# Performance work log

Hardware: AMD Instinct MI355X
Metric: run time of the kernel (lower is better)

## Reference

```python
import jax, jax.numpy as jnp
import numpy as np

K = 5  # kNN neighbors (includes self, as in PyG knn(x, x, k))


def _lin_bn(x, W, b, s, h):
    # Linear -> ReLU -> BatchNorm (inference, folded to scale s / shift h)
    return jax.nn.relu(x @ W + b) * s + h


def _knn_idx(x, k):
    # x: [B, N, F] -> idx: [B, N, k] indices of k nearest points (incl. self)
    x2 = jnp.sum(x * x, axis=-1)  # [B, N]
    d = x2[:, :, None] + x2[:, None, :] - 2.0 * jnp.einsum('bnf,bmf->bnm', x, x)
    return jax.lax.top_k(-d, k)[1]


def _edge_conv(x, k, edge_mlp):
    # DynamicEdgeConv: knn graph, message mlp([x_i, x_j - x_i]), max-aggregate
    idx = _knn_idx(x, k)                                   # [B, N, k]
    xj = jax.vmap(lambda xb, ib: xb[ib])(x, idx)           # [B, N, k, F]
    xi = jnp.broadcast_to(x[:, :, None, :], xj.shape)
    e = jnp.concatenate([xi, xj - xi], axis=-1)            # [B, N, k, 2F]
    return jnp.max(edge_mlp(e), axis=2)                    # [B, N, F_out]


def _forward(pos, w1a, b1a, s1a, h1a, w1b, b1b, s1b, h1b, w1c, b1c, s1c, h1c,
             w2, b2, s2, h2, wl, bl, sl, hl,
             wm1, bm1, sm1, hm1, wm2, bm2, sm2, hm2, wout, bout):
    mlp1 = lambda e: _lin_bn(_lin_bn(_lin_bn(e, w1a, b1a, s1a, h1a),
                                     w1b, b1b, s1b, h1b), w1c, b1c, s1c, h1c)
    mlp2 = lambda e: _lin_bn(e, w2, b2, s2, h2)
    x1 = _edge_conv(pos, K, mlp1)                          # [B, N, 64]
    x2 = _edge_conv(x1, K, mlp2)                           # [B, N, 128]
    out = _lin_bn(jnp.concatenate([x1, x2], axis=-1), wl, bl, sl, hl)  # [B,N,1024]
    out = jnp.max(out, axis=1)                             # global max pool -> [B,1024]
    out = _lin_bn(out, wm1, bm1, sm1, hm1)                 # Dropout = identity (eval)
    out = _lin_bn(out, wm2, bm2, sm2, hm2)
    return out @ wout + bout                               # [B, n_classes]


def setup_inputs() -> dict:
    key = jax.random.key(0)
    ks = jax.random.split(key, 32)
    B, N = 32, 2048
    rn = lambda k, sh: jax.random.normal(k, sh, dtype=jnp.float32)
    ru = lambda k, sh: jax.random.uniform(k, sh, dtype=jnp.float32)
    d = {'pos': rn(ks[0], (B, N, 3))}
    i = 1
    for nm, cin, cout in [('1a', 6, 64), ('1b', 64, 64), ('1c', 64, 64),
                          ('2', 128, 128), ('l', 192, 1024),
                          ('m1', 1024, 512), ('m2', 512, 256)]:
        d['w' + nm] = rn(ks[i], (cin, cout)) / np.sqrt(cin); i += 1
        d['b' + nm] = rn(ks[i], (cout,)) * 0.1; i += 1
        d['s' + nm] = ru(ks[i], (cout,)) + 0.5; i += 1
        d['h' + nm] = rn(ks[i], (cout,)) * 0.1; i += 1
    d['wout'] = rn(ks[i], (256, 2)) / np.sqrt(256.0); i += 1
    d['bout'] = rn(ks[i], (2,)) * 0.1
    return d


def reference(pos, w1a, b1a, s1a, h1a, w1b, b1b, s1b, h1b, w1c, b1c, s1c, h1c,
              w2, b2, s2, h2, wl, bl, sl, hl,
              wm1, bm1, sm1, hm1, wm2, bm2, sm2, hm2, wout, bout):
    return _forward(pos, w1a, b1a, s1a, h1a, w1b, b1b, s1b, h1b, w1c, b1c, s1c, h1c,
                    w2, b2, s2, h2, wl, bl, sl, hl,
                    wm1, bm1, sm1, hm1, wm2, bm2, sm2, hm2, wout, bout)
```

## Files before the change

### kernel.cpp

```cpp
#include <hip/hip_runtime.h>

#define DEV __device__ __forceinline__
DEV float relu_(float x) { return fmaxf(x, 0.0f); }

typedef __attribute__((ext_vector_type(4))) float f32x4;
typedef __attribute__((ext_vector_type(8))) __bf16 bf16x8;

DEV unsigned short bfbits(__bf16 b) { union { unsigned short s; __bf16 b; } x; x.b = b; return x.s; }
DEV __bf16 bffrom(unsigned short s) { union { unsigned short s; __bf16 b; } x; x.s = s; return x.b; }

DEV void knn_insert(float (&bd)[5], int (&bi)[5], float d, int j) {
  if (d >= bd[4]) return;
  bd[4] = d; bi[4] = j;
#pragma unroll
  for (int p = 4; p > 0; --p) {
    if (bd[p] < bd[p - 1]) {
      float td = bd[p]; bd[p] = bd[p - 1]; bd[p - 1] = td;
      int ti = bi[p]; bi[p] = bi[p - 1]; bi[p - 1] = ti;
    }
  }
}

DEV void knn_insert_bl(float (&bd)[5], int (&bi)[5], float d, int j) {
#pragma unroll
  for (int p = 0; p < 5; ++p) {
    bool lt = d < bd[p];
    float nd = lt ? d : bd[p];
    float cd = lt ? bd[p] : d;
    int ni = lt ? j : bi[p];
    int ci = lt ? bi[p] : j;
    bd[p] = nd; d = cd;
    bi[p] = ni; j = ci;
  }
}

DEV void ins5(float (&b)[5], float x) {
  b[4] = __builtin_amdgcn_fmed3f(b[3], b[4], x);
  b[3] = __builtin_amdgcn_fmed3f(b[2], b[3], x);
  b[2] = __builtin_amdgcn_fmed3f(b[1], b[2], x);
  b[1] = __builtin_amdgcn_fmed3f(b[0], b[1], x);
  b[0] = fminf(b[0], x);
}

__global__ __launch_bounds__(256) void k_front(
    const float* __restrict__ pos, const float* __restrict__ w1a,
    const float* __restrict__ b1a, const float* __restrict__ w1b,
    const float* __restrict__ w1c, const float* __restrict__ w2,
    const float* __restrict__ wl,
    int* __restrict__ idx1, float* __restrict__ uR, float* __restrict__ vR,
    __bf16* __restrict__ wfh, __bf16* __restrict__ wfl,
    __bf16* __restrict__ wph, __bf16* __restrict__ wpl,
    __bf16* __restrict__ wlb) {
  __shared__ __align__(16) float smem[9472];
  int tid = threadIdx.x;
  int blk = blockIdx.x;
  if (blk < 2048) {
    float* ps = smem;
    float* sqs = smem + 6144;
    float* md = smem + 8192;
    int* mi = (int*)(smem + 8832);
    int b = blk >> 6, qc = blk & 63;
    const float* src = pos + b * 6144;
    for (int u = tid; u < 6144; u += 256) ps[u] = src[u];
    __syncthreads();
    for (int u = tid; u < 2048; u += 256) {
      float x = ps[u * 3], y = ps[u * 3 + 1], z = ps[u * 3 + 2];
      sqs[u] = fmaf(z, z, fmaf(y, y, x * x));
    }
    __syncthreads();
    int q = tid & 31, sub = tid >> 5;
    int qi = qc * 32 + q;
    float qx = ps[qi * 3], qy = ps[qi * 3 + 1], qz = ps[qi * 3 + 2];
    float qsq = sqs[qi];
    float bp[5] = {1e30f, 1e30f, 1e30f, 1e30f, 1e30f};
    int j0 = sub * 256;
    for (int j = j0; j < j0 + 256; ++j) {
      float px = ps[j * 3], py = ps[j * 3 + 1], pz = ps[j * 3 + 2];
      float dot = fmaf(qz, pz, fmaf(qy, py, qx * px));
      float d = fmaxf((qsq + sqs[j]) - 2.0f * dot, 0.0f);
      unsigned u = (__float_as_uint(d) & 0xFFFFFF00u) | (unsigned)(j & 255);
      ins5(bp, __uint_as_float(u));
    }
    float bd[5]; int bi[5];
#pragma unroll
    for (int k = 0; k < 5; ++k) {
      unsigned u = __float_as_uint(bp[k]);
      bd[k] = __uint_as_float(u & 0xFFFFFF00u);
      bi[k] = j0 + (int)(u & 255u);
    }
    for (int half = 4; half >= 1; half >>= 1) {
      __syncthreads();
      if (sub >= half && sub < 2 * half) {
        int slot = (q * 4 + (sub - half)) * 5;
#pragma unroll
        for (int k = 0; k < 5; ++k) { md[slot + k] = bd[k]; mi[slot + k] = bi[k]; }
      }
      __syncthreads();
      if (sub < half) {
        int slot = (q * 4 + sub) * 5;
#pragma unroll
        for (int k = 0; k < 5; ++k) knn_insert_bl(bd, bi, md[slot + k], mi[slot + k]);
      }
    }
    if (sub == 0) {
      int* op = idx1 + (b * 2048 + qi) * 5;
#pragma unroll
      for (int k = 0; k < 5; ++k) op[k] = bi[k];
    }
  } else if (blk < 3072) {
    float* wAs = smem;
    float* bs = smem + 384;
    float* uS = smem + 448;
    float* vS = smem + 4800;
    for (int u = tid; u < 384; u += 256) wAs[u] = w1a[u];
    if (tid < 64) bs[tid] = b1a[tid];
    __syncthreads();
    int lane = tid & 63, fq = tid >> 6;
    int p0 = (blk - 2048) * 64;
    int p = p0 + lane;
    float x0 = pos[p * 3], x1 = pos[p * 3 + 1], x2 = pos[p * 3 + 2];
#pragma unroll
    for (int m = 0; m < 16; ++m) {
      int f = fq * 16 + m;
      float wt0 = wAs[f], wt1 = wAs[64 + f], wt2 = wAs[128 + f];
      float wb0 = wAs[192 + f], wb1 = wAs[256 + f], wb2 = wAs[320 + f];
      float uval = bs[f];
      uval = fmaf(x0, wt0 - wb0, uval);
      uval = fmaf(x1, wt1 - wb1, uval);
      uval = fmaf(x2, wt2 - wb2, uval);
      uS[lane * 68 + f] = uval;
      vS[lane * 68 + f] = fmaf(x2, wb2, fmaf(x1, wb1, x0 * wb0));
    }
    __syncthreads();
#pragma unroll
    for (int it = 0; it < 4; ++it) {
      int g = it * 1024 + tid * 4;
      int pl = g >> 6, f = g & 63;
      float4 uu = *(const float4*)(uS + pl * 68 + f);
      float4 vv = *(const float4*)(vS + pl * 68 + f);
      *(float4*)(uR + (size_t)p0 * 64 + g) = uu;
      *(float4*)(vR + (size_t)p0 * 64 + g) = vv;
    }
  } else {
    int pblk = blk - 3072;
    if (pblk < 4) {
      int t = pblk * 256 + tid;
      int m = t >> 9;
      int rem = t & 511;
      int nb = rem >> 7;
      int rem2 = rem & 127;
      int s = rem2 >> 6, lane = rem2 & 63;
      int k0 = s * 32 + (lane >> 4) * 8;
      int c = nb * 16 + (lane & 15);
      const float* W = m ? w1c : w1b;
      __bf16 oh[8], ol[8];
#pragma unroll
      for (int j = 0; j < 8; ++j) {
        float val = W[(k0 + j) * 64 + c];
        __bf16 h = (__bf16)val;
        oh[j] = h;
        ol[j] = (__bf16)(val - (float)h);
      }
      size_t off = (size_t)m * 4096 + ((size_t)((nb * 2 + s) * 64 + lane)) * 8;
      *(uint4*)(wfh + off) = *(const uint4*)oh;
      *(uint4*)(wfl + off) = *(const uint4*)ol;
    } else if (pblk < 12) {
      int t = (pblk - 4) * 256 + tid;
      int nb = t >> 7;
      int rem = t & 127;
      int ks = rem >> 6, lane = rem & 63;
      int k0 = ks * 32 + (lane >> 4) * 8;
      int col16 = lane & 15;
      __bf16 oh[8], ol[8];
#pragma unroll
      for (int j = 0; j < 8; ++j) {
        int k = k0 + j;
        float val;
        if (nb < 8) {
          int c = nb * 16 + col16;
          val = w2[k * 128 + c] - w2[(64 + k) * 128 + c];
        } else {
          int c = (nb - 8) * 16 + col16;
          val = w2[(64 + k) * 128 + c];
        }
        __bf16 h = (__bf16)val;
        oh[j] = h;
        ol[j] = (__bf16)(val - (float)h);
      }
      *(uint4*)(wph + (size_t)t * 8) = *(const uint4*)oh;
      *(uint4*)(wpl + (size_t)t * 8) = *(const uint4*)ol;
    } else {
      int t = (pblk - 12) * 256 + tid;
      int nt = t / 3072;
      int rem = t - nt * 3072;
      int ks = rem / 512;
      int rem2 = rem - ks * 512;
      int nb = rem2 >> 6, lane = rem2 & 63;
      int k0 = ks * 32 + (lane >> 4) * 8;
      int n = nt * 128 + nb * 16 + (lane & 15);
      __bf16 o[8];
#pragma unroll
      for (int j = 0; j < 8; ++j) o[j] = (__bf16)wl[(k0 + j) * 1024 + n];
      *(uint4*)(wlb + (size_t)t * 8) = *(const uint4*)o;
    }
  }
}

__global__ __launch_bounds__(256) void k_edge1(
    const int* __restrict__ idx1, const float* __restrict__ uR,
    const float* __restrict__ vR,
    const float* __restrict__ s1a, const float* __restrict__ h1a,
    const float* __restrict__ b1b, const float* __restrict__ s1b,
    const float* __restrict__ h1b,
    const float* __restrict__ b1c, const float* __restrict__ s1c,
    const float* __restrict__ h1c,
    const __bf16* __restrict__ wfh, const __bf16* __restrict__ wfl,
    __bf16* __restrict__ xh, __bf16* __restrict__ xl,
    float* __restrict__ sqo, __bf16* __restrict__ xb) {
  __shared__ __align__(16) __bf16 Wh[8192], Wl[8192];
  __shared__ __align__(16) unsigned h2b[4 * 1088];
  int tid = threadIdx.x;
  int w = tid >> 6, lane = tid & 63;
  int quad = lane >> 4, lm = lane & 15;
#pragma unroll
  for (int it = 0; it < 4; ++it) {
    int u4 = it * 256 + tid;
    *(uint4*)(Wh + (size_t)u4 * 8) = *(const uint4*)(wfh + (size_t)u4 * 8);
    *(uint4*)(Wl + (size_t)u4 * 8) = *(const uint4*)(wfl + (size_t)u4 * 8);
  }
  int p0 = blockIdx.x * 64;
  int b = p0 >> 11;
  size_t bb = (size_t)b * 2048;
  int edge = p0 + w * 16 + lm;
  float sA[2][8], hA[2][8];
#pragma unroll
  for (int s = 0; s < 2; ++s)
#pragma unroll
    for (int j = 0; j < 8; ++j) {
      int k = s * 32 + quad * 8 + j;
      sA[s][j] = s1a[k]; hA[s][j] = h1a[k];
    }
  float bB[4], sB[4], hB[4], bC[4], sC[4], hC[4];
#pragma unroll
  for (int nb = 0; nb < 4; ++nb) {
    int c = nb * 16 + lm;
    bB[nb] = b1b[c]; sB[nb] = s1b[c]; hB[nb] = h1b[c];
    bC[nb] = b1c[c]; sC[nb] = s1c[c]; hC[nb] = h1c[c];
  }
  unsigned* h2w = h2b + w * 1088;
  f32x4 mmax[4];
#pragma unroll
  for (int nb = 0; nb < 4; ++nb)
    mmax[nb] = (f32x4){-3.4e38f, -3.4e38f, -3.4e38f, -3.4e38f};
  __syncthreads();
  const float* urow = uR + (size_t)edge * 64;
  for (int kk = 0; kk < 5; ++kk) {
    int jn = idx1[edge * 5 + kk];
    const float* vrow = vR + (bb + jn) * 64;
    bf16x8 Ah[2], Al[2];
#pragma unroll
    for (int s = 0; s < 2; ++s) {
      int off = s * 32 + quad * 8;
      float4 u0 = *(const float4*)(urow + off);
      float4 u1 = *(const float4*)(urow + off + 4);
      float4 v0 = *(const float4*)(vrow + off);
      float4 v1 = *(const float4*)(vrow + off + 4);
      float uv[8] = {u0.x + v0.x, u0.y + v0.y, u0.z + v0.z, u0.w + v0.w,
                     u1.x + v1.x, u1.y + v1.y, u1.z + v1.z, u1.w + v1.w};
      __bf16 th[8], tl[8];
#pragma unroll
      for (int j = 0; j < 8; ++j) {
        float val = relu_(uv[j]) * sA[s][j] + hA[s][j];
        __bf16 hb = (__bf16)val;
        th[j] = hb;
        tl[j] = (__bf16)(val - (float)hb);
      }
      Ah[s] = *(const bf16x8*)th;
      Al[s] = *(const bf16x8*)tl;
    }
#pragma unroll
    for (int nb = 0; nb < 4; ++nb) {
      bf16x8 Bh0 = *(const bf16x8*)(Wh + ((size_t)((nb * 2 + 0) * 64 + lane)) * 8);
      bf16x8 Bh1 = *(const bf16x8*)(Wh + ((size_t)((nb * 2 + 1) * 64 + lane)) * 8);
      bf16x8 Bl0 = *(const bf16x8*)(Wl + ((size_t)((nb * 2 + 0) * 64 + lane)) * 8);
      bf16x8 Bl1 = *(const bf16x8*)(Wl + ((size_t)((nb * 2 + 1) * 64 + lane)) * 8);
      f32x4 a2 = {0.f, 0.f, 0.f, 0.f};
      a2 = __builtin_amdgcn_mfma_f32_16x16x32_bf16(Ah[0], Bh0, a2, 0, 0, 0);
      a2 = __builtin_amdgcn_mfma_f32_16x16x32_bf16(Ah[1], Bh1, a2, 0, 0, 0);
      a2 = __builtin_amdgcn_mfma_f32_16x16x32_bf16(Ah[0], Bl0, a2, 0, 0, 0);
      a2 = __builtin_amdgcn_mfma_f32_16x16x32_bf16(Ah[1], Bl1, a2, 0, 0, 0);
      a2 = __builtin_amdgcn_mfma_f32_16x16x32_bf16(Al[0], Bh0, a2, 0, 0, 0);
      a2 = __builtin_amdgcn_mfma_f32_16x16x32_bf16(Al[1], Bh1, a2, 0, 0, 0);
#pragma unroll
      for (int r = 0; r < 4; ++r) {
        float vv2 = relu_(a2[r] + bB[nb]) * sB[nb] + hB[nb];
        __bf16 hb = (__bf16)vv2;
        __bf16 lb = (__bf16)(vv2 - (float)hb);
        h2w[(quad * 4 + r) * 68 + nb * 16 + lm] =
            (unsigned)bfbits(hb) | ((unsigned)bfbits(lb) << 16);
      }
    }
    bf16x8 A3h[2], A3l[2];
#pragma unroll
    for (int s = 0; s < 2; ++s) {
      const unsigned* rp = h2w + lm * 68 + s * 32 + quad * 8;
      uint4 da = *(const uint4*)rp;
      uint4 db = *(const uint4*)(rp + 4);
      unsigned dw[8] = {da.x, da.y, da.z, da.w, db.x, db.y, db.z, db.w};
      __bf16 th[8], tl[8];
#pragma unroll
      for (int j = 0; j < 8; ++j) {
        th[j] = bffrom((unsigned short)(dw[j] & 0xFFFFu));
        tl[j] = bffrom((unsigned short)(dw[j] >> 16));
      }
      A3h[s] = *(const bf16x8*)th;
      A3l[s] = *(const bf16x8*)tl;
    }
#pragma unroll
    for (int nb = 0; nb < 4; ++nb) {
      bf16x8 Bh0 = *(const bf16x8*)(Wh + 4096 + ((size_t)((nb * 2 + 0) * 64 + lane)) * 8);
      bf16x8 Bh1 = *(const bf16x8*)(Wh + 4096 + ((size_t)((nb * 2 + 1) * 64 + lane)) * 8);
      bf16x8 Bl0 = *(const bf16x8*)(Wl + 4096 + ((size_t)((nb * 2 + 0) * 64 + lane)) * 8);
      bf16x8 Bl1 = *(const bf16x8*)(Wl + 4096 + ((size_t)((nb * 2 + 1) * 64 + lane)) * 8);
      f32x4 a3 = {0.f, 0.f, 0.f, 0.f};
      a3 = __builtin_amdgcn_mfma_f32_16x16x32_bf16(A3h[0], Bh0, a3, 0, 0, 0);
      a3 = __builtin_amdgcn_mfma_f32_16x16x32_bf16(A3h[1], Bh1, a3, 0, 0, 0);
      a3 = __builtin_amdgcn_mfma_f32_16x16x32_bf16(A3h[0], Bl0, a3, 0, 0, 0);
      a3 = __builtin_amdgcn_mfma_f32_16x16x32_bf16(A3h[1], Bl1, a3, 0, 0, 0);
      a3 = __builtin_amdgcn_mfma_f32_16x16x32_bf16(A3l[0], Bh0, a3, 0, 0, 0);
      a3 = __builtin_amdgcn_mfma_f32_16x16x32_bf16(A3l[1], Bh1, a3, 0, 0, 0);
#pragma unroll
      for (int r = 0; r < 4; ++r) mmax[nb][r] = fmaxf(mmax[nb][r], a3[r]);
    }
  }
  float sqp[4] = {0.f, 0.f, 0.f, 0.f};
#pragma unroll
  for (int nb = 0; nb < 4; ++nb) {
    int c = nb * 16 + lm;
#pragma unroll
    for (int r = 0; r < 4; ++r) {
      float vv3 = relu_(mmax[nb][r] + bC[nb]) * sC[nb] + hC[nb];
      sqp[r] = fmaf(vv3, vv3, sqp[r]);
      __bf16 hb = (__bf16)vv3;
      __bf16 lb = (__bf16)(vv3 - (float)hb);
      int n = p0 + w * 16 + quad * 4 + r;
      xh[(size_t)n * 64 + c] = hb;
      xl[(size_t)n * 64 + c] = lb;
      xb[(size_t)n * 192 + c] = hb;
    }
  }
#pragma unroll
  for (int r = 0; r < 4; ++r) {
    float s = sqp[r];
    s += __shfl_xor(s, 1);
    s += __shfl_xor(s, 2);
    s += __shfl_xor(s, 4);
    s += __shfl_xor(s, 8);
    if (lm == 0) sqo[p0 + w * 16 + quad * 4 + r] = s;
  }
}

__global__ __launch_bounds__(256) void k_mid(const __bf16* __restrict__ xh,
                                             const __bf16* __restrict__ xl,
                                             const float* __restrict__ sq,
                                             int* __restrict__ idx2,
                                             const __bf16* __restrict__ wph,
                                             const __bf16* __restrict__ wpl,
                                             __bf16* __restrict__ Pb,
                                             __bf16* __restrict__ Qb) {
  __shared__ __align__(16) float smem[6656];
  int tid = threadIdx.x;
  int w = tid >> 6, lane = tid & 63;
  int quad = lane >> 4, lm = lane & 15;
  if (blockIdx.x < 1024) {
    __bf16* Bh = (__bf16*)smem;
    __bf16* Bl = (__bf16*)(smem + 2304);
    float* sqs = smem + 4608;
    int b = blockIdx.x >> 5, qc = blockIdx.x & 31;
    int q0 = qc * 64;
    size_t bb = (size_t)b * 2048;
    for (int u = tid; u < 512; u += 256)
      *(float4*)(sqs + u * 4) = *(const float4*)(sq + bb + u * 4);
    const __bf16* qh = xh + (bb + q0 + w * 16 + lm) * 64 + quad * 8;
    const __bf16* ql = xl + (bb + q0 + w * 16 + lm) * 64 + quad * 8;
    bf16x8 Ah0 = *(const bf16x8*)(qh);
    bf16x8 Ah1 = *(const bf16x8*)(qh + 32);
    bf16x8 Al0 = *(const bf16x8*)(ql);
    bf16x8 Al1 = *(const bf16x8*)(ql + 32);
    __syncthreads();
    float qsq[4];
#pragma unroll
    for (int r = 0; r < 4; ++r) qsq[r] = sqs[q0 + w * 16 + quad * 4 + r];
    float bp[4][5];
#pragma unroll
    for (int r = 0; r < 4; ++r)
#pragma unroll
      for (int k = 0; k < 5; ++k) bp[r][k] = 1e30f;
    for (int ct = 0; ct < 32; ++ct) {
#pragma unroll
      for (int pass = 0; pass < 2; ++pass) {
        int unit = pass * 256 + tid;
        int n = unit >> 3, cc = unit & 7;
        const __bf16* gsrc = xh + (bb + ct * 64 + n) * 64 + cc * 8;
        const __bf16* gsrl = xl + (bb + ct * 64 + n) * 64 + cc * 8;
        *(uint4*)(Bh + n * 72 + cc * 8) = *(const uint4*)gsrc;
        *(uint4*)(Bl + n * 72 + cc * 8) = *(const uint4*)gsrl;
      }
      __syncthreads();
#pragma unroll
      for (int nt = 0; nt < 4; ++nt) {
        const __bf16* bph = Bh + (nt * 16 + lm) * 72 + quad * 8;
        const __bf16* bpl = Bl + (nt * 16 + lm) * 72 + quad * 8;
        bf16x8 Bh0 = *(const bf16x8*)(bph);
        bf16x8 Bh1 = *(const bf16x8*)(bph + 32);
        bf16x8 Bl0 = *(const bf16x8*)(bpl);
        bf16x8 Bl1 = *(const bf16x8*)(bpl + 32);
        f32x4 acc = {0.f, 0.f, 0.f, 0.f};
        acc = __builtin_amdgcn_mfma_f32_16x16x32_bf16(Ah0, Bh0, acc, 0, 0, 0);
        acc = __builtin_amdgcn_mfma_f32_16x16x32_bf16(Ah1, Bh1, acc, 0, 0, 0);
        acc = __builtin_amdgcn_mfma_f32_16x16x32_bf16(Ah0, Bl0, acc, 0, 0, 0);
        acc = __builtin_amdgcn_mfma_f32_16x16x32_bf16(Ah1, Bl1, acc, 0, 0, 0);
        acc = __builtin_amdgcn_mfma_f32_16x16x32_bf16(Al0, Bh0, acc, 0, 0, 0);
        acc = __builtin_amdgcn_mfma_f32_16x16x32_bf16(Al1, Bh1, acc, 0, 0, 0);
        int cid = ct * 64 + nt * 16 + lm;
        float csq = sqs[cid];
        unsigned key = (unsigned)(ct * 4 + nt);
#pragma unroll
        for (int r = 0; r < 4; ++r) {
          float d = fmaxf((qsq[r] + csq) - 2.0f * acc[r], 0.0f);
          unsigned u = (__float_as_uint(d) & 0xFFFFFF80u) | key;
          ins5(bp[r], __uint_as_float(u));
        }
      }
      __syncthreads();
    }
    float bd[4][5];
    int bi[4][5];
#pragma unroll
    for (int r = 0; r < 4; ++r)
#pragma unroll
      for (int k = 0; k < 5; ++k) {
        unsigned u = __float_as_uint(bp[r][k]);
        bd[r][k] = __uint_as_float(u & 0xFFFFFF80u);
        bi[r][k] = (int)((u & 0x7Fu) << 4) | lm;
      }
    for (int m = 1; m <= 8; m <<= 1) {
#pragma unroll
      for (int r = 0; r < 4; ++r) {
        float od[5]; int oi[5];
#pragma unroll
        for (int k = 0; k < 5; ++k) {
          od[k] = __shfl_xor(bd[r][k], m);
          oi[k] = __shfl_xor(bi[r][k], m);
        }
#pragma unroll
        for (int k = 0; k < 5; ++k) knn_insert(bd[r], bi[r], od[k], oi[k]);
      }
    }
    if (lm == 0) {
#pragma unroll
      for (int r = 0; r < 4; ++r) {
        int qi = q0 + w * 16 + quad * 4 + r;
        int* op = idx2 + (bb + qi) * 5;
#pragma unroll
        for (int k = 0; k < 5; ++k) op[k] = bi[r][k];
      }
    }
  } else {
    __bf16* Wh = (__bf16*)smem;
    __bf16* Wl = (__bf16*)(smem + 2048);
    int n0 = (blockIdx.x - 1024) * 64;
    const __bf16* ah = xh + (size_t)(n0 + w * 16 + lm) * 64 + quad * 8;
    const __bf16* al = xl + (size_t)(n0 + w * 16 + lm) * 64 + quad * 8;
    bf16x8 Ah0 = *(const bf16x8*)(ah);
    bf16x8 Ah1 = *(const bf16x8*)(ah + 32);
    bf16x8 Al0 = *(const bf16x8*)(al);
    bf16x8 Al1 = *(const bf16x8*)(al + 32);
    for (int chunk = 0; chunk < 4; ++chunk) {
      __syncthreads();
#pragma unroll
      for (int it = 0; it < 2; ++it) {
        int unit = it * 256 + tid;
        *(uint4*)(Wh + (size_t)unit * 8) =
            *(const uint4*)(wph + (size_t)chunk * 4096 + (size_t)unit * 8);
        *(uint4*)(Wl + (size_t)unit * 8) =
            *(const uint4*)(wpl + (size_t)chunk * 4096 + (size_t)unit * 8);
      }
      __syncthreads();
#pragma unroll
      for (int nb4 = 0; nb4 < 4; ++nb4) {
        int nb = chunk * 4 + nb4;
        bf16x8 Bh0 = *(const bf16x8*)(Wh + ((size_t)(nb4 * 2 + 0) * 64 + lane) * 8);
        bf16x8 Bh1 = *(const bf16x8*)(Wh + ((size_t)(nb4 * 2 + 1) * 64 + lane) * 8);
        bf16x8 Bl0 = *(const bf16x8*)(Wl + ((size_t)(nb4 * 2 + 0) * 64 + lane) * 8);
        bf16x8 Bl1 = *(const bf16x8*)(Wl + ((size_t)(nb4 * 2 + 1) * 64 + lane) * 8);
        f32x4 acc = {0.f, 0.f, 0.f, 0.f};
        acc = __builtin_amdgcn_mfma_f32_16x16x32_bf16(Ah0, Bh0, acc, 0, 0, 0);
        acc = __builtin_amdgcn_mfma_f32_16x16x32_bf16(Ah1, Bh1, acc, 0, 0, 0);
        acc = __builtin_amdgcn_mfma_f32_16x16x32_bf16(Ah0, Bl0, acc, 0, 0, 0);
        acc = __builtin_amdgcn_mfma_f32_16x16x32_bf16(Ah1, Bl1, acc, 0, 0, 0);
        acc = __builtin_amdgcn_mfma_f32_16x16x32_bf16(Al0, Bh0, acc, 0, 0, 0);
        acc = __builtin_amdgcn_mfma_f32_16x16x32_bf16(Al1, Bh1, acc, 0, 0, 0);
        bool isP = (nb < 8);
        __bf16* base = isP ? Pb : Qb;
        int col = (isP ? nb : nb - 8) * 16 + lm;
#pragma unroll
        for (int r = 0; r < 4; ++r) {
          int n = n0 + w * 16 + quad * 4 + r;
          base[(size_t)n * 128 + col] = (__bf16)acc[r];
        }
      }
    }
  }
}

__global__ __launch_bounds__(256) void k_gmax(const __bf16* __restrict__ Pb,
                                              const __bf16* __restrict__ Qb,
                                              const int* __restrict__ idx2,
                                              const float* __restrict__ b2,
                                              const float* __restrict__ s2,
                                              const float* __restrict__ h2v,
                                              __bf16* __restrict__ xb) {
  int tid = threadIdx.x;
  int c4 = tid & 31, p = tid >> 5;
  int n = blockIdx.x * 8 + p;
  int b = n >> 11;
  const int* ip = idx2 + n * 5;
  int c0 = c4 * 4;
  float m[4] = {-3.4e38f, -3.4e38f, -3.4e38f, -3.4e38f};
#pragma unroll
  for (int k = 0; k < 5; ++k) {
    int j = ip[k];
    uint2 q = *(const uint2*)(Qb + ((size_t)(b * 2048 + j)) * 128 + c0);
    m[0] = fmaxf(m[0], (float)bffrom((unsigned short)(q.x & 0xFFFFu)));
    m[1] = fmaxf(m[1], (float)bffrom((unsigned short)(q.x >> 16)));
    m[2] = fmaxf(m[2], (float)bffrom((unsigned short)(q.y & 0xFFFFu)));
    m[3] = fmaxf(m[3], (float)bffrom((unsigned short)(q.y >> 16)));
  }
  uint2 pv = *(const uint2*)(Pb + (size_t)n * 128 + c0);
  float pvf[4] = {(float)bffrom((unsigned short)(pv.x & 0xFFFFu)),
                  (float)bffrom((unsigned short)(pv.x >> 16)),
                  (float)bffrom((unsigned short)(pv.y & 0xFFFFu)),
                  (float)bffrom((unsigned short)(pv.y >> 16))};
  __bf16 o[4];
#pragma unroll
  for (int i = 0; i < 4; ++i) {
    float v = pvf[i] + m[i] + b2[c0 + i];
    o[i] = (__bf16)(relu_(v) * s2[c0 + i] + h2v[c0 + i]);
  }
  uint2 ov;
  ov.x = (unsigned)bfbits(o[0]) | ((unsigned)bfbits(o[1]) << 16);
  ov.y = (unsigned)bfbits(o[2]) | ((unsigned)bfbits(o[3]) << 16);
  *(uint2*)(xb + (size_t)n * 192 + 64 + c0) = ov;
}

__global__ __launch_bounds__(256) void k_linl_mfma(const __bf16* __restrict__ xb,
                                                   const __bf16* __restrict__ wlb,
                                                   float* __restrict__ pool_part) {
  __shared__ __align__(16) __bf16 Aall[12288];
  __shared__ __align__(16) __bf16 Bl[8192];
  int tid = threadIdx.x;
  int w = tid >> 6, lane = tid & 63;
  int mg = blockIdx.x;
  int n0 = mg << 6;
  int quad = lane >> 4, lm = lane & 15;
#pragma unroll
  for (int it = 0; it < 6; ++it) {
    int unit = it * 256 + tid;
    int mb = unit / 384;
    int rem = unit - mb * 384;
    int ks = rem >> 6, ln = rem & 63;
    int lmm = ln & 15, qd = ln >> 4;
    const uint4* ga = (const uint4*)(xb + (size_t)(n0 + mb * 16 + lmm) * 192 + ks * 32 + qd * 8);
    *(uint4*)(Aall + ((size_t)(mb * 6 + ks) * 64 + ln) * 8) = *ga;
  }
  for (int ng = 0; ng < 4; ++ng) {
    f32x4 acc[4][4];
#pragma unroll
    for (int i = 0; i < 4; ++i)
#pragma unroll
      for (int j = 0; j < 4; ++j) acc[i][j] = (f32x4){0.f, 0.f, 0.f, 0.f};
    for (int ks = 0; ks < 6; ++ks) {
      __syncthreads();
#pragma unroll
      for (int nt2 = 0; nt2 < 2; ++nt2) {
#pragma unroll
        for (int u = 0; u < 2; ++u) {
          int unit = u * 256 + tid;
          const uint4* gb = (const uint4*)(wlb + ((size_t)((ng * 2 + nt2) * 6 + ks)) * 4096 + (size_t)unit * 8);
          *(uint4*)(Bl + (size_t)nt2 * 4096 + (size_t)unit * 8) = *gb;
        }
      }
      __syncthreads();
      bf16x8 af[4], bfr[4];
#pragma unroll
      for (int i = 0; i < 4; ++i)
        af[i] = *(const bf16x8*)(Aall + ((size_t)(i * 6 + ks) * 64 + lane) * 8);
      int nt2 = w >> 1, nbb = (w & 1) * 4;
#pragma unroll
      for (int j = 0; j < 4; ++j)
        bfr[j] = *(const bf16x8*)(Bl + (size_t)nt2 * 4096 + ((size_t)((nbb + j) * 64 + lane)) * 8);
#pragma unroll
      for (int i = 0; i < 4; ++i)
#pragma unroll
        for (int j = 0; j < 4; ++j)
          acc[i][j] = __builtin_amdgcn_mfma_f32_16x16x32_bf16(af[i], bfr[j], acc[i][j], 0, 0, 0);
    }
#pragma unroll
    for (int j = 0; j < 4; ++j) {
      float m = -3.4e38f;
#pragma unroll
      for (int i = 0; i < 4; ++i)
#pragma unroll
        for (int r = 0; r < 4; ++r) m = fmaxf(m, acc[i][j][r]);
      m = fmaxf(m, __shfl_xor(m, 16));
      m = fmaxf(m, __shfl_xor(m, 32));
      if (quad == 0) {
        int ch = ng * 256 + (w >> 1) * 128 + (w & 1) * 64 + j * 16 + lm;
        pool_part[(size_t)mg * 1024 + ch] = m;
      }
    }
  }
}

__global__ __launch_bounds__(256) void k_head(
    const float* __restrict__ pool_part, const float* __restrict__ bl,
    const float* __restrict__ sl, const float* __restrict__ hl,
    const float* __restrict__ wm1, const float* __restrict__ bm1,
    const float* __restrict__ sm1, const float* __restrict__ hm1,
    const float* __restrict__ wm2, const float* __restrict__ bm2,
    const float* __restrict__ sm2, const float* __restrict__ hm2,
    const float* __restrict__ wout, const float* __restrict__ bout,
    float* __restrict__ out) {
  __shared__ float p_s[1024], h1_s[512], h2_s[256];
  int b = blockIdx.x, tid = threadIdx.x;
  for (int c = tid; c < 1024; c += 256) {
    float m = -3.4e38f;
#pragma unroll 4
    for (int t = 0; t < 32; ++t)
      m = fmaxf(m, pool_part[(size_t)(b * 32 + t) * 1024 + c]);
    p_s[c] = relu_(m + bl[c]) * sl[c] + hl[c];
  }
  __syncthreads();
  for (int c = tid; c < 512; c += 256) {
    float a0 = 0, a1 = 0, a2 = 0, a3 = 0;
    for (int f = 0; f < 1024; f += 4) {
      a0 = fmaf(p_s[f], wm1[f * 512 + c], a0);
      a1 = fmaf(p_s[f + 1], wm1[(f + 1) * 512 + c], a1);
      a2 = fmaf(p_s[f + 2], wm1[(f + 2) * 512 + c], a2);
      a3 = fmaf(p_s[f + 3], wm1[(f + 3) * 512 + c], a3);
    }
    float a = (a0 + a1) + (a2 + a3);
    h1_s[c] = relu_(a + bm1[c]) * sm1[c] + hm1[c];
  }
  __syncthreads();
  if (tid < 256) {
    float a0 = 0, a1 = 0, a2 = 0, a3 = 0;
    for (int f = 0; f < 512; f += 4) {
      a0 = fmaf(h1_s[f], wm2[f * 256 + tid], a0);
      a1 = fmaf(h1_s[f + 1], wm2[(f + 1) * 256 + tid], a1);
      a2 = fmaf(h1_s[f + 2], wm2[(f + 2) * 256 + tid], a2);
      a3 = fmaf(h1_s[f + 3], wm2[(f + 3) * 256 + tid], a3);
    }
    float a = (a0 + a1) + (a2 + a3);
    h2_s[tid] = relu_(a + bm2[tid]) * sm2[tid] + hm2[tid];
  }
  __syncthreads();
  if (tid < 2) {
    float a0 = 0, a1 = 0;
    for (int f = 0; f < 256; f += 2) {
      a0 = fmaf(h2_s[f], wout[f * 2 + tid], a0);
      a1 = fmaf(h2_s[f + 1], wout[(f + 1) * 2 + tid], a1);
    }
    out[b * 2 + tid] = (a0 + a1) + bout[tid];
  }
}

extern "C" void kernel_launch(void* const* d_in, const int* in_sizes, int n_in,
                              void* d_out, int out_size, void* d_ws, size_t ws_size,
                              hipStream_t stream) {
  const float* pos = (const float*)d_in[0];
  const float* w1a = (const float*)d_in[1];
  const float* b1a = (const float*)d_in[2];
  const float* s1a = (const float*)d_in[3];
  const float* h1a = (const float*)d_in[4];
  const float* w1b = (const float*)d_in[5];
  const float* b1b = (const float*)d_in[6];
  const float* s1b = (const float*)d_in[7];
  const float* h1b = (const float*)d_in[8];
  const float* w1c = (const float*)d_in[9];
  const float* b1c = (const float*)d_in[10];
  const float* s1c = (const float*)d_in[11];
  const float* h1c = (const float*)d_in[12];
  const float* w2 = (const float*)d_in[13];
  const float* b2 = (const float*)d_in[14];
  const float* s2 = (const float*)d_in[15];
  const float* h2 = (const float*)d_in[16];
  const float* wl = (const float*)d_in[17];
  const float* bl = (const float*)d_in[18];
  const float* sl = (const float*)d_in[19];
  const float* hl = (const float*)d_in[20];
  const float* wm1 = (const float*)d_in[21];
  const float* bm1 = (const float*)d_in[22];
  const float* sm1 = (const float*)d_in[23];
  const float* hm1 = (const float*)d_in[24];
  const float* wm2 = (const float*)d_in[25];
  const float* bm2 = (const float*)d_in[26];
  const float* sm2 = (const float*)d_in[27];
  const float* hm2 = (const float*)d_in[28];
  const float* wout = (const float*)d_in[29];
  const float* bout = (const float*)d_in[30];
  float* out = (float*)d_out;

  float* base = (float*)d_ws;
  __bf16* xh = (__bf16*)base;
  __bf16* xl = (__bf16*)(base + 2097152);
  float* PbF = base + 4194304;
  float* QbF = PbF + 4194304;
  float* xbF = QbF + 4194304;
  int* idx = (int*)(xbF + 6291456);
  float* sq = (float*)(idx + 327680);
  __bf16* wph = (__bf16*)(sq + 65536);
  __bf16* wpl = (__bf16*)(sq + 65536 + 8192);
  __bf16* wfh = (__bf16*)(sq + 65536 + 16384);
  __bf16* wfl = (__bf16*)(sq + 65536 + 20480);
  __bf16* wlb = (__bf16*)(sq + 65536 + 24576);
  __bf16* Pb = (__bf16*)PbF;
  __bf16* Qb = (__bf16*)QbF;
  __bf16* xb = (__bf16*)xbF;
  float* uR = PbF;
  float* vR = QbF;
  float* pool_part = base + 131072;

  k_front<<<3180, 256, 0, stream>>>(pos, w1a, b1a, w1b, w1c, w2, wl, idx, uR, vR,
                                    wfh, wfl, wph, wpl, wlb);
  k_edge1<<<1024, 256, 0, stream>>>(idx, uR, vR, s1a, h1a, b1b, s1b, h1b, b1c,
                                    s1c, h1c, wfh, wfl, xh, xl, sq, xb);
  k_mid<<<2048, 256, 0, stream>>>(xh, xl, sq, idx, wph, wpl, Pb, Qb);
  k_gmax<<<8192, 256, 0, stream>>>(Pb, Qb, idx, b2, s2, h2, xb);
  k_linl_mfma<<<1024, 256, 0, stream>>>(xb, wlb, pool_part);
  k_head<<<32, 256, 0, stream>>>(pool_part, bl, sl, hl, wm1, bm1, sm1, hm1, wm2,
                                 bm2, sm2, hm2, wout, bout, out);
}
```

Baseline: 434.3 us.

## Split head MLP into three kernels with more blocks and split-K reductions

Replaces the single 32-block head kernel, which serially ran the pool reduction and the dense layers per batch, with three kernels. k_pool, k_m1 and k_m2o split channels across many blocks and split the K dimension across warps, combining partials through a shared-memory reduction. The final 256x2 layer is fused into k_m2o using wave shuffles and atomicAdd into an output that k_pool zeroes. This spreads the latency-bound head across more CUs, at the cost of two extra launches and atomics whose summation order is nondeterministic.

```diff
diff --git a/kernel.cpp b/kernel.cpp
--- a/kernel.cpp
+++ b/kernel.cpp
@@ -623,56 +623,101 @@
   }
 }
 
-__global__ __launch_bounds__(256) void k_head(
-    const float* __restrict__ pool_part, const float* __restrict__ bl,
-    const float* __restrict__ sl, const float* __restrict__ hl,
-    const float* __restrict__ wm1, const float* __restrict__ bm1,
-    const float* __restrict__ sm1, const float* __restrict__ hm1,
-    const float* __restrict__ wm2, const float* __restrict__ bm2,
-    const float* __restrict__ sm2, const float* __restrict__ hm2,
-    const float* __restrict__ wout, const float* __restrict__ bout,
-    float* __restrict__ out) {
-  __shared__ float p_s[1024], h1_s[512], h2_s[256];
-  int b = blockIdx.x, tid = threadIdx.x;
-  for (int c = tid; c < 1024; c += 256) {
-    float m = -3.4e38f;
-#pragma unroll 4
-    for (int t = 0; t < 32; ++t)
-      m = fmaxf(m, pool_part[(size_t)(b * 32 + t) * 1024 + c]);
-    p_s[c] = relu_(m + bl[c]) * sl[c] + hl[c];
-  }
+__global__ __launch_bounds__(256) void k_pool(const float* __restrict__ pool_part,
+                                              const float* __restrict__ bl,
+                                              const float* __restrict__ sl,
+                                              const float* __restrict__ hl,
+                                              float* __restrict__ p,
+                                              float* __restrict__ out) {
+  int b = blockIdx.x >> 2, cb = blockIdx.x & 3;
+  int c = cb * 256 + threadIdx.x;
+  const float* src = pool_part + (size_t)(b * 32) * 1024 + c;
+  float m0 = -3.4e38f, m1 = -3.4e38f, m2 = -3.4e38f, m3 = -3.4e38f;
+#pragma unroll
+  for (int t = 0; t < 32; t += 4) {
+    m0 = fmaxf(m0, src[(size_t)t * 1024]);
+    m1 = fmaxf(m1, src[(size_t)(t + 1) * 1024]);
+    m2 = fmaxf(m2, src[(size_t)(t + 2) * 1024]);
+    m3 = fmaxf(m3, src[(size_t)(t + 3) * 1024]);
+  }
+  float m = fmaxf(fmaxf(m0, m1), fmaxf(m2, m3));
+  p[b * 1024 + c] = relu_(m + bl[c]) * sl[c] + hl[c];
+  if (blockIdx.x == 0 && threadIdx.x < 64) out[threadIdx.x] = 0.0f;
+}
+
+__global__ __launch_bounds__(256) void k_m1(const float* __restrict__ p,
+                                            const float* __restrict__ wm1,
+                                            const float* __restrict__ bm1,
+                                            const float* __restrict__ sm1,
+                                            const float* __restrict__ hm1,
+                                            float* __restrict__ h1) {
+  __shared__ float p_s[1024];
+  __shared__ float red[4][64];
+  int b = blockIdx.x >> 3, cb = blockIdx.x & 7;
+  int tid = threadIdx.x;
+  for (int u = tid; u < 1024; u += 256) p_s[u] = p[b * 1024 + u];
   __syncthreads();
-  for (int c = tid; c < 512; c += 256) {
-    float a0 = 0, a1 = 0, a2 = 0, a3 = 0;
-    for (int f = 0; f < 1024; f += 4) {
-      a0 = fmaf(p_s[f], wm1[f * 512 + c], a0);
-      a1 = fmaf(p_s[f + 1], wm1[(f + 1) * 512 + c], a1);
-      a2 = fmaf(p_s[f + 2], wm1[(f + 2) * 512 + c], a2);
-      a3 = fmaf(p_s[f + 3], wm1[(f + 3) * 512 + c], a3);
-    }
-    float a = (a0 + a1) + (a2 + a3);
-    h1_s[c] = relu_(a + bm1[c]) * sm1[c] + hm1[c];
-  }
+  int c64 = tid & 63, q = tid >> 6;
+  int C = cb * 64 + c64;
+  int f0 = q * 256;
+  const float* W = wm1 + (size_t)f0 * 512 + C;
+  float a[8] = {0.f, 0.f, 0.f, 0.f, 0.f, 0.f, 0.f, 0.f};
+  for (int f = 0; f < 256; f += 8) {
+#pragma unroll
+    for (int u = 0; u < 8; ++u)
+      a[u] = fmaf(p_s[f0 + f + u], W[(size_t)(f + u) * 512], a[u]);
+  }
+  red[q][c64] = ((a[0] + a[1]) + (a[2] + a[3])) + ((a[4] + a[5]) + (a[6] + a[7]));
   __syncthreads();
-  if (tid < 256) {
-    float a0 = 0, a1 = 0, a2 = 0, a3 = 0;
-    for (int f = 0; f < 512; f += 4) {
-      a0 = fmaf(h1_s[f], wm2[f * 256 + tid], a0);
-      a1 = fmaf(h1_s[f + 1], wm2[(f + 1) * 256 + tid], a1);
-      a2 = fmaf(h1_s[f + 2], wm2[(f + 2) * 256 + tid], a2);
-      a3 = fmaf(h1_s[f + 3], wm2[(f + 3) * 256 + tid], a3);
-    }
-    float a = (a0 + a1) + (a2 + a3);
-    h2_s[tid] = relu_(a + bm2[tid]) * sm2[tid] + hm2[tid];
-  }
+  if (tid < 64) {
+    float t = (red[0][tid] + red[1][tid]) + (red[2][tid] + red[3][tid]);
+    int C2 = cb * 64 + tid;
+    h1[b * 512 + C2] = relu_(t + bm1[C2]) * sm1[C2] + hm1[C2];
+  }
+}
+
+__global__ __launch_bounds__(256) void k_m2o(const float* __restrict__ h1,
+                                             const float* __restrict__ wm2,
+                                             const float* __restrict__ bm2,
+                                             const float* __restrict__ sm2,
+                                             const float* __restrict__ hm2,
+                                             const float* __restrict__ wout,
+                                             const float* __restrict__ bout,
+                                             float* __restrict__ out) {
+  __shared__ float h1_s[512];
+  __shared__ float red[4][64];
+  int b = blockIdx.x >> 2, cb = blockIdx.x & 3;
+  int tid = threadIdx.x;
+  for (int u = tid; u < 512; u += 256) h1_s[u] = h1[b * 512 + u];
   __syncthreads();
-  if (tid < 2) {
-    float a0 = 0, a1 = 0;
-    for (int f = 0; f < 256; f += 2) {
-      a0 = fmaf(h2_s[f], wout[f * 2 + tid], a0);
-      a1 = fmaf(h2_s[f + 1], wout[(f + 1) * 2 + tid], a1);
-    }
-    out[b * 2 + tid] = (a0 + a1) + bout[tid];
+  int c64 = tid & 63, q = tid >> 6;
+  int C = cb * 64 + c64;
+  int f0 = q * 128;
+  const float* W = wm2 + (size_t)f0 * 256 + C;
+  float a[4] = {0.f, 0.f, 0.f, 0.f};
+  for (int f = 0; f < 128; f += 4) {
+#pragma unroll
+    for (int u = 0; u < 4; ++u)
+      a[u] = fmaf(h1_s[f0 + f + u], W[(size_t)(f + u) * 256], a[u]);
+  }
+  red[q][c64] = (a[0] + a[1]) + (a[2] + a[3]);
+  __syncthreads();
+  if (tid < 64) {
+    float t = (red[0][tid] + red[1][tid]) + (red[2][tid] + red[3][tid]);
+    int C2 = cb * 64 + tid;
+    float h2v = relu_(t + bm2[C2]) * sm2[C2] + hm2[C2];
+    float2 wv = *(const float2*)(wout + C2 * 2);
+    float v0 = h2v * wv.x, v1 = h2v * wv.y;
+#pragma unroll
+    for (int m = 1; m < 64; m <<= 1) {
+      v0 += __shfl_xor(v0, m);
+      v1 += __shfl_xor(v1, m);
+    }
+    if (tid == 0) {
+      if (cb == 0) { v0 += bout[0]; v1 += bout[1]; }
+      atomicAdd(&out[b * 2], v0);
+      atomicAdd(&out[b * 2 + 1], v1);
+    }
   }
 }
 
@@ -731,6 +776,8 @@
   float* uR = PbF;
   float* vR = QbF;
   float* pool_part = base + 131072;
+  float* p_pool = base + 1179648;
+  float* h1g = base + 1212416;
 
   k_front<<<3180, 256, 0, stream>>>(pos, w1a, b1a, w1b, w1c, w2, wl, idx, uR, vR,
                                     wfh, wfl, wph, wpl, wlb);
@@ -739,6 +786,7 @@
   k_mid<<<2048, 256, 0, stream>>>(xh, xl, sq, idx, wph, wpl, Pb, Qb);
   k_gmax<<<8192, 256, 0, stream>>>(Pb, Qb, idx, b2, s2, h2, xb);
   k_linl_mfma<<<1024, 256, 0, stream>>>(xb, wlb, pool_part);
-  k_head<<<32, 256, 0, stream>>>(pool_part, bl, sl, hl, wm1, bm1, sm1, hm1, wm2,
-                                 bm2, sm2, hm2, wout, bout, out);
-}
+  k_pool<<<128, 256, 0, stream>>>(pool_part, bl, sl, hl, p_pool, out);
+  k_m1<<<256, 256, 0, stream>>>(p_pool, wm1, bm1, sm1, hm1, h1g);
+  k_m2o<<<128, 256, 0, stream>>>(h1g, wm2, bm2, sm2, hm2, wout, bout, out);
+}
```

Measured after the change: 358.8 us. -17.4%, faster.
